# Optimization experiments

Hardware: AMD Instinct MI355X
Metric: run time of the kernel (lower is better)

Reference implementation:

```python
import jax, jax.numpy as jnp
import numpy as np

# SSD300 common_params
MAP_SIZES = np.array([38, 19, 10, 5, 3, 1])
NUM_BOXES = np.array([4, 6, 6, 6, 4, 4])
NUM_OFFSET = 4
LOC_VAR = 0.1
NUM_CLASSES = 21
NEG_POS_RATIO = 3
_counts = MAP_SIZES ** 2 * NUM_BOXES
LAYER_OFFSETS = np.concatenate([[0], np.cumsum(_counts)])[:6]
TOTAL_ANCHORS = int(_counts.sum())  # 8732

B, MAXGT, SEG_HW = 32, 64, 300


def setup_inputs() -> dict:
    key = jax.random.key(0)
    ks = jax.random.split(key, 6)
    rng = np.random.default_rng(0)
    layer = rng.integers(0, 6, (B, MAXGT))
    pos = rng.integers(0, MAP_SIZES[layer] ** 2)
    dbox = rng.integers(0, NUM_BOXES[layer])
    nvalid = rng.integers(8, MAXGT + 1, (B,))
    live = np.arange(MAXGT)[None, :] < nvalid[:, None]
    layer = np.where(live, layer, -100)  # -100 sentinel terminates per-image list
    idx_batch = jnp.asarray(np.stack([np.zeros_like(layer), layer, pos, dbox], -1), dtype=jnp.int64)
    cls_batch = jnp.asarray(rng.integers(1, NUM_CLASSES, (B, MAXGT)), dtype=jnp.int64)
    return {
        "Loc": jax.random.normal(ks[0], (B, TOTAL_ANCHORS, NUM_OFFSET), jnp.float32),
        "Cls": jax.random.normal(ks[1], (B, TOTAL_ANCHORS, NUM_CLASSES), jnp.float32),
        "Seg": jax.random.normal(ks[2], (B, NUM_CLASSES, SEG_HW, SEG_HW), jnp.float32),
        "gt_box_batch": jax.random.uniform(ks[3], (B, MAXGT, NUM_OFFSET), jnp.float32),
        "df_box_batch": jax.random.uniform(ks[4], (B, MAXGT, NUM_OFFSET), jnp.float32),
        "idx_batch": idx_batch,
        "cls_batch": cls_batch,
        "bat_s": B,
        "mining": 1,
        "seg_label": jax.random.randint(ks[5], (B, SEG_HW, SEG_HW), 0, NUM_CLASSES, jnp.int64),
    }


def _build_targets(idx_batch, cls_batch, gt_box_batch, df_box_batch, mining):
    # Vectorized replacement of the nested scalar-scatter loop.
    layer = idx_batch[..., 1]
    fpos = idx_batch[..., 2]
    dbox = idx_batch[..., 3]
    # original loop breaks at first -100: mask everything after it
    valid = jnp.cumprod((layer != -100).astype(jnp.int32), axis=1).astype(bool)
    lc = jnp.clip(layer, 0, 5)
    offs = jnp.asarray(LAYER_OFFSETS)[lc]
    nb = jnp.asarray(NUM_BOXES)[lc]
    # [B, num_boxes, H, W] permuted to [B, H, W, num_boxes] -> flat = pos*nb + dbox
    flat = offs + fpos * nb + dbox
    flat = jnp.where(valid, flat, TOTAL_ANCHORS)  # dump slot
    bsz = idx_batch.shape[0]
    b_idx = jnp.arange(bsz)[:, None]
    init = -1 if mining else 0
    cls_t = jnp.full((bsz, TOTAL_ANCHORS + 1), init, dtype=jnp.int32)
    cls_t = cls_t.at[b_idx, flat].set(jnp.where(valid, cls_batch.astype(jnp.int32), init))
    delta = (gt_box_batch - df_box_batch) / LOC_VAR
    loc_t = jnp.zeros((bsz, TOTAL_ANCHORS + 1, NUM_OFFSET), jnp.float32)
    loc_t = loc_t.at[b_idx, flat].set(jnp.where(valid[..., None], delta, 0.0))
    return cls_t[:, :TOTAL_ANCHORS], loc_t[:, :TOTAL_ANCHORS]


def _mt_loss(Loc, Cls, Seg, gt_box_batch, df_box_batch, idx_batch, cls_batch, mining, seg_label):
    cls_t, loc_t = _build_targets(idx_batch, cls_batch, gt_box_batch, df_box_batch, mining)
    pos = cls_t > 0
    num_pos = jnp.maximum(pos.sum(), 1).astype(jnp.float32)
    logp = jax.nn.log_softmax(Cls, axis=-1)  # [B,N,C]
    ce = -jnp.take_along_axis(logp, jnp.clip(cls_t, 0, NUM_CLASSES - 1)[..., None].astype(jnp.int32), axis=-1)[..., 0]
    loss_cls_pos = jnp.where(pos, ce, 0.0).sum()
    if mining:
        # hard negative mining: top (3*num_pos_i) background losses per image
        ce_bg = -logp[..., 0]
        neg_cand = cls_t == -1
        scores = jnp.where(neg_cand, ce_bg, -jnp.inf)
        order = jnp.argsort(-scores, axis=1)
        rank = jnp.argsort(order, axis=1)
        num_pos_i = pos.sum(axis=1, keepdims=True)
        num_neg_i = jnp.minimum(NEG_POS_RATIO * num_pos_i, neg_cand.sum(axis=1, keepdims=True))
        sel = neg_cand & (rank < num_neg_i)
        loss_cls_neg = jnp.where(sel, ce_bg, 0.0).sum()
    else:
        # all non-positive anchors are explicit background targets (cls_t == 0)
        loss_cls_neg = jnp.where(~pos, ce, 0.0).sum()
    loss_cls = (loss_cls_pos + loss_cls_neg) / num_pos
    d = Loc - loc_t
    ad = jnp.abs(d)
    sl1 = jnp.where(ad < 1.0, 0.5 * d * d, ad - 0.5)
    loss_loc = jnp.where(pos[..., None], sl1, 0.0).sum() / num_pos
    seg_logp = jax.nn.log_softmax(Seg, axis=1)  # [B,C,H,W]
    seg_ce = -jnp.take_along_axis(seg_logp, seg_label[:, None].astype(jnp.int32), axis=1)[:, 0]
    loss_seg = seg_ce.mean()
    return loss_cls + loss_loc + loss_seg


def reference(Loc, Cls, Seg, gt_box_batch, df_box_batch, idx_batch, cls_batch, bat_s, mining, seg_label):
    return _mt_loss(Loc, Cls, Seg, gt_box_batch, df_box_batch, idx_batch, cls_batch, mining, seg_label)
```

## Files before the change

kernel.cpp:

```cpp
#include <hip/hip_runtime.h>
#include <stdint.h>

#define BATCH 32
#define NA 8732
#define NC 21
#define SHW 90000
#define MAXGT 64
#define NQ (SHW / 4)

#define SPI 8
#define SQUADS 2816
#define QPT 11
#define WQ 704
#define CHBF (SQUADS * 4)
#define CSTEP ((size_t)NQ * 16)

__constant__ int c_loff[6] = {0, 5776, 7942, 8542, 8692, 8728};
__constant__ int c_lnb[6]  = {4, 6, 6, 6, 4, 4};

__device__ __forceinline__ unsigned f2key(float f) {
    unsigned u = __float_as_uint(f);
    return (u & 0x80000000u) ? ~u : (u | 0x80000000u);
}
__device__ __forceinline__ float key2f(unsigned k) {
    return __uint_as_float((k & 0x80000000u) ? (k ^ 0x80000000u) : ~k);
}

__global__ __launch_bounds__(64) void k_init(float* __restrict__ acc, int* __restrict__ npt,
                                             unsigned* __restrict__ done) {
    int t = threadIdx.x;
    if (t < 8) acc[t] = 0.0f;
    if (t == 8) *npt = 0;
    if (t == 9) *done = 0u;
}

__global__ __launch_bounds__(1024) void k_build(
    const int* __restrict__ idxb, const int* __restrict__ clsb,
    const float* __restrict__ gt, const float* __restrict__ df,
    const float* __restrict__ Loc, const int* __restrict__ mining_p,
    signed char* __restrict__ cls_t, float* __restrict__ acc,
    int* __restrict__ num_pos_i, int* __restrict__ neg_cnt_i,
    int* __restrict__ npt)
{
    const int b = blockIdx.x;
    const int tid = threadIdx.x;
    __shared__ int s_flat[MAXGT];
    __shared__ int s_cls[MAXGT];
    __shared__ float s_delta[MAXGT][4];
    __shared__ int s_nv;
    __shared__ float s_wf[16];
    __shared__ int s_wp[16];
    __shared__ int s_wn[16];

    if (tid < MAXGT) {
        int layer = idxb[(b * MAXGT + tid) * 4 + 1];
        int fpos  = idxb[(b * MAXGT + tid) * 4 + 2];
        int dbox  = idxb[(b * MAXGT + tid) * 4 + 3];
        int fl;
        if (layer == -100) fl = -2;
        else {
            int lc = min(max(layer, 0), 5);
            fl = c_loff[lc] + fpos * c_lnb[lc] + dbox;
        }
        s_flat[tid] = fl;
        s_cls[tid] = clsb[b * MAXGT + tid];
        #pragma unroll
        for (int o = 0; o < 4; o++)
            s_delta[tid][o] = (gt[(b * MAXGT + tid) * 4 + o] - df[(b * MAXGT + tid) * 4 + o]) / 0.1f;
    }
    __syncthreads();
    if (tid == 0) {
        int nv = MAXGT;
        for (int j = 0; j < MAXGT; j++) if (s_flat[j] == -2) { nv = j; break; }
        s_nv = nv;
    }
    __syncthreads();
    const int nv = s_nv;

    int rflat[MAXGT];
    #pragma unroll
    for (int j = 0; j < MAXGT; j++)
        rflat[j] = (j < nv) ? s_flat[j] : -3;

    const int mining = *mining_p;
    const signed char cinit = mining ? (signed char)(-1) : (signed char)0;
    int pos_cnt = 0, neg_cnt = 0;
    float loc_sum = 0.0f;

    for (int a = tid; a < NA; a += 1024) {
        int best = -1;
        #pragma unroll
        for (int j = 0; j < MAXGT; j++)
            best = (rflat[j] == a) ? j : best;
        signed char cv = cinit;
        if (best >= 0) cv = (signed char)s_cls[best];
        cls_t[b * NA + a] = cv;
        if (cv > 0) {
            pos_cnt++;
            const float4 l4 = *reinterpret_cast<const float4*>(Loc + ((size_t)b * NA + a) * 4);
            float lv[4] = {l4.x, l4.y, l4.z, l4.w};
            #pragma unroll
            for (int o = 0; o < 4; o++) {
                float d = lv[o] - s_delta[best][o];
                float ad = fabsf(d);
                loc_sum += (ad < 1.0f) ? (0.5f * d * d) : (ad - 0.5f);
            }
        } else if (cv == -1) {
            neg_cnt++;
        }
    }

    #pragma unroll
    for (int d = 32; d > 0; d >>= 1) {
        loc_sum += __shfl_down(loc_sum, d);
        pos_cnt += __shfl_down(pos_cnt, d);
        neg_cnt += __shfl_down(neg_cnt, d);
    }
    const int lane = tid & 63, wv = tid >> 6;
    if (lane == 0) { s_wf[wv] = loc_sum; s_wp[wv] = pos_cnt; s_wn[wv] = neg_cnt; }
    __syncthreads();
    if (tid == 0) {
        float lf = 0.0f; int pp = 0, nn = 0;
        #pragma unroll
        for (int w = 0; w < 16; w++) { lf += s_wf[w]; pp += s_wp[w]; nn += s_wn[w]; }
        atomicAdd(acc + 2, lf);
        num_pos_i[b] = pp;
        atomicAdd(npt, pp);
        neg_cnt_i[b] = nn;
    }
}

__global__ __launch_bounds__(256) void k_cls(
    const float* __restrict__ Cls, const signed char* __restrict__ cls_t,
    const int* __restrict__ mining_p, float* __restrict__ scores,
    float* __restrict__ acc)
{
    __shared__ __align__(16) float s_c[256 * NC];
    __shared__ float s_wp[4];
    __shared__ float s_wn[4];
    const int t = threadIdx.x;
    const size_t base = (size_t)blockIdx.x * (256 * NC);
    const size_t total = (size_t)BATCH * NA * NC;
    const int nchunks = (int)((total - base) >> 2) < (256 * NC / 4)
                        ? (int)((total - base) >> 2) : (256 * NC / 4);
    #pragma unroll
    for (int k = 0; k < 6; k++) {
        int j4 = t + k * 256;
        if (j4 < nchunks) {
            *reinterpret_cast<float4*>(&s_c[j4 * 4]) =
                *reinterpret_cast<const float4*>(Cls + base + (size_t)j4 * 4);
        }
    }
    __syncthreads();

    const int r = blockIdx.x * 256 + t;
    const int mining = *mining_p;
    float pos_ce = 0.0f, neg_ce = 0.0f;
    if (r < BATCH * NA) {
        float f[NC];
        #pragma unroll
        for (int c = 0; c < NC; c++) f[c] = s_c[t * NC + c];
        float m = f[0];
        #pragma unroll
        for (int c = 1; c < NC; c++) m = fmaxf(m, f[c]);
        float s = 0.0f;
        #pragma unroll
        for (int c = 0; c < NC; c++) s += __expf(f[c] - m);
        float lse = m + __logf(s);
        int ct = (int)cls_t[r];
        int lab = ct > 0 ? ct : 0;
        float xt = f[0];
        #pragma unroll
        for (int c = 1; c < NC; c++) xt = (c == lab) ? f[c] : xt;
        float ce_bg = lse - f[0];
        if (ct > 0) pos_ce = lse - xt;
        if (mining) {
            scores[r] = (ct == -1) ? ce_bg : -__builtin_inff();
        } else if (ct <= 0) {
            neg_ce = ce_bg;
        }
    }
    #pragma unroll
    for (int d = 32; d > 0; d >>= 1) {
        pos_ce += __shfl_down(pos_ce, d);
        neg_ce += __shfl_down(neg_ce, d);
    }
    const int lane = t & 63, wv = t >> 6;
    if (lane == 0) { s_wp[wv] = pos_ce; s_wn[wv] = neg_ce; }
    __syncthreads();
    if (t == 0) {
        float p = s_wp[0] + s_wp[1] + s_wp[2] + s_wp[3];
        float n = s_wn[0] + s_wn[1] + s_wn[2] + s_wn[3];
        if (p != 0.0f) atomicAdd(acc + 0, p);
        if (n != 0.0f) atomicAdd(acc + 1, n);
    }
}

__global__ __launch_bounds__(256) void k_topk(
    const float* __restrict__ scores, const int* __restrict__ num_pos_i,
    const int* __restrict__ neg_cnt_i, const int* __restrict__ mining_p,
    float* __restrict__ acc)
{
    if (*mining_p == 0) return;
    const int b = blockIdx.x;
    const int tid = threadIdx.x;
    const int k = min(3 * num_pos_i[b], neg_cnt_i[b]);
    if (k <= 0) return;

    __shared__ unsigned s_keys[NA];
    __shared__ int s_hist[256];
    __shared__ int s_wsum[4];
    __shared__ int s_selb;
    __shared__ int s_sele;
    __shared__ float s_wf[4];
    __shared__ int s_wc[4];

    const float* sc = scores + (size_t)b * NA;
    for (int a = tid; a < NA; a += 256)
        s_keys[a] = f2key(sc[a]);

    const int lane = tid & 63, wv = tid >> 6;
    unsigned pref = 0u;
    int k_rem = k;

    #pragma unroll
    for (int lvl = 0; lvl < 4; lvl++) {
        const int sh = 24 - lvl * 8;
        s_hist[tid] = 0;
        __syncthreads();
        for (int a = tid; a < NA; a += 256) {
            unsigned key = s_keys[a];
            bool in = (lvl == 0) || ((key >> (sh + 8)) == pref);
            if (in) atomicAdd(&s_hist[(key >> sh) & 0xFF], 1);
        }
        __syncthreads();
        const int b_rev = 255 - tid;
        const int v = s_hist[b_rev];
        int x = v;
        #pragma unroll
        for (int d = 1; d < 64; d <<= 1) {
            int o = __shfl_up(x, d);
            if (lane >= d) x += o;
        }
        if (lane == 63) s_wsum[wv] = x;
        __syncthreads();
        for (int w = 0; w < wv; w++) x += s_wsum[w];
        if (x >= k_rem && (x - v) < k_rem) { s_selb = b_rev; s_sele = x - v; }
        __syncthreads();
        pref = (pref << 8) | (unsigned)s_selb;
        k_rem -= s_sele;
        __syncthreads();
    }

    float sum_g = 0.0f; int cnt_g = 0;
    for (int a = tid; a < NA; a += 256) {
        unsigned key = s_keys[a];
        if (key > pref) { sum_g += key2f(key); cnt_g++; }
    }
    #pragma unroll
    for (int d = 32; d > 0; d >>= 1) {
        sum_g += __shfl_down(sum_g, d);
        cnt_g += __shfl_down(cnt_g, d);
    }
    if (lane == 0) { s_wf[wv] = sum_g; s_wc[wv] = cnt_g; }
    __syncthreads();
    if (tid == 0) {
        float sg = s_wf[0] + s_wf[1] + s_wf[2] + s_wf[3];
        int cg = s_wc[0] + s_wc[1] + s_wc[2] + s_wc[3];
        atomicAdd(acc + 1, sg + (float)(k - cg) * key2f(pref));
    }
}


__device__ __forceinline__ void upd1(float& m, float& s, float& tg,
                                     int lab, float x, int c) {
    tg = (lab == c) ? x : tg;
    const float d = x - m;
    const float e = __expf(-fabsf(d));
    s = (d > 0.0f) ? fmaf(s, e, 1.0f) : (s + e);
    m = fmaxf(m, x);
}
__device__ __forceinline__ void upd4p(float4& m, float4& s, float4& tg,
                                      unsigned lp, const float4& x, int c) {
    upd1(m.x, s.x, tg.x, (int)(lp & 0xFFu),         x.x, c);
    upd1(m.y, s.y, tg.y, (int)((lp >> 8) & 0xFFu),  x.y, c);
    upd1(m.z, s.z, tg.z, (int)((lp >> 16) & 0xFFu), x.z, c);
    upd1(m.w, s.w, tg.w, (int)((lp >> 24) & 0xFFu), x.w, c);
}

#define GLOAD_I4(dst, addr) \
    asm volatile("global_load_dwordx4 %0, %1, off" : "=v"(dst) : "v"(addr))
#define SWAIT(lit) do { \
    asm volatile("s_waitcnt vmcnt(" #lit ")" ::: "memory"); \
    __builtin_amdgcn_sched_barrier(0); } while (0)

__device__ __forceinline__ void stage_chan(const char* segbase, int c,
                                           float* ldswave, const uint32_t* boff) {
    const char* cb = segbase + (size_t)c * CSTEP;
    #pragma unroll
    for (int i = 0; i < QPT; i++) {
        __builtin_amdgcn_global_load_lds(
            (__attribute__((address_space(1))) void*)(cb + boff[i]),
            (__attribute__((address_space(3))) void*)(ldswave + i * 256),
            16, 0, 0);
    }
}

#define RBAR() do { \
    __builtin_amdgcn_sched_barrier(0); \
    __builtin_amdgcn_s_barrier(); \
    __builtin_amdgcn_sched_barrier(0); } while (0)

__global__ __launch_bounds__(256, 1) void k_seg(
    const float* __restrict__ Seg, const int* __restrict__ slab_lab,
    float* __restrict__ acc, const int* __restrict__ npt,
    unsigned* __restrict__ done, float* __restrict__ out)
{
    __shared__ __align__(16) float s_buf[3 * CHBF];
    __shared__ float s_w[4];
    const int t = threadIdx.x;
    const int lane = t & 63, w = t >> 6;
    const int img = blockIdx.x >> 3;
    const int sl  = blockIdx.x & 7;
    const int qbase = sl * SQUADS;

    const char* segbase = (const char*)(Seg + (size_t)img * NC * SHW);
    const char* labbase = (const char*)(slab_lab + (size_t)img * SHW);

    int4 la[QPT];
    #pragma unroll
    for (int k = 0; k < QPT; k++) {
        int q = qbase + t + k * 256;
        int qc = (q < NQ) ? q : (NQ - 1);
        GLOAD_I4(la[k], (uint64_t)labbase + (uint64_t)qc * 16u);
    }
    SWAIT(0);
    unsigned lp[QPT];
    #pragma unroll
    for (int k = 0; k < QPT; k++)
        lp[k] = ((unsigned)la[k].x & 0xFFu) | (((unsigned)la[k].y & 0xFFu) << 8)
              | (((unsigned)la[k].z & 0xFFu) << 16) | (((unsigned)la[k].w & 0xFFu) << 24);

    uint32_t boff[QPT];
    #pragma unroll
    for (int i = 0; i < QPT; i++) {
        int qg = qbase + w * WQ + i * 64 + lane;
        int qc = (qg < NQ) ? qg : (NQ - 1);
        boff[i] = (uint32_t)qc * 16u;
    }
    float* ldsw0 = s_buf + (size_t)w * (WQ * 4);

    float4 m4[QPT], s4[QPT], t4[QPT];

    stage_chan(segbase, 0, ldsw0, boff);
    stage_chan(segbase, 1, ldsw0 + CHBF, boff);
    SWAIT(11);
    RBAR();
    stage_chan(segbase, 2, ldsw0 + 2 * CHBF, boff);
    #pragma unroll
    for (int k = 0; k < QPT; k++) {
        float4 x = *reinterpret_cast<const float4*>(s_buf + (size_t)(t + k * 256) * 4);
        m4[k] = x; t4[k] = x;
        s4[k] = make_float4(1.f, 1.f, 1.f, 1.f);
    }

    #pragma unroll 1
    for (int c = 1; c < NC; ++c) {
        if (c == NC - 1) SWAIT(0); else SWAIT(11);
        RBAR();
        if (c + 2 < NC) stage_chan(segbase, c + 2, ldsw0 + ((c + 2) % 3) * CHBF, boff);
        const float* bp = s_buf + (size_t)(c % 3) * CHBF;
        #pragma unroll
        for (int k = 0; k < QPT; k++) {
            float4 x = *reinterpret_cast<const float4*>(bp + (size_t)(t + k * 256) * 4);
            upd4p(m4[k], s4[k], t4[k], lp[k], x, c);
        }
    }

    float lsum = 0.0f;
    #pragma unroll
    for (int k = 0; k < QPT; k++) {
        int q = qbase + t + k * 256;
        if (q < NQ) {
            lsum += (m4[k].x + __logf(s4[k].x) - t4[k].x)
                  + (m4[k].y + __logf(s4[k].y) - t4[k].y)
                  + (m4[k].z + __logf(s4[k].z) - t4[k].z)
                  + (m4[k].w + __logf(s4[k].w) - t4[k].w);
        }
    }

    #pragma unroll
    for (int d = 32; d > 0; d >>= 1) lsum += __shfl_down(lsum, d);
    if (lane == 0) s_w[w] = lsum;
    __syncthreads();
    if (t == 0) {
        atomicAdd(acc + 3, s_w[0] + s_w[1] + s_w[2] + s_w[3]);
        __threadfence();
        unsigned old = atomicAdd(done, 1u);
        if (old == gridDim.x - 1) {
            __threadfence();
            int np_i = *npt;
            float np = (float)(np_i > 1 ? np_i : 1);
            out[0] = (acc[0] + acc[1] + acc[2]) / np
                   + acc[3] / (float)(BATCH * SHW);
        }
    }
}

extern "C" void kernel_launch(void* const* d_in, const int* in_sizes, int n_in,
                              void* d_out, int out_size, void* d_ws, size_t ws_size,
                              hipStream_t stream)
{
    const float* Loc = (const float*)d_in[0];
    const float* Cls = (const float*)d_in[1];
    const float* Seg = (const float*)d_in[2];
    const float* gt  = (const float*)d_in[3];
    const float* df  = (const float*)d_in[4];
    const int* idxb  = (const int*)d_in[5];
    const int* clsb  = (const int*)d_in[6];
    const int* mining_p = (const int*)d_in[8];
    const int* slab  = (const int*)d_in[9];
    float* out = (float*)d_out;

    char* ws = (char*)d_ws;
    float* acc        = (float*)ws;
    int*   npt        = (int*)(ws + 32);
    unsigned* done    = (unsigned*)(ws + 36);
    int*   num_pos_i  = (int*)(ws + 64);
    int*   neg_cnt_i  = (int*)(ws + 192);
    signed char* cls_t = (signed char*)(ws + 512);
    float* scores      = (float*)(ws + 512 + 279424);

    hipLaunchKernelGGL(k_init, dim3(1), dim3(64), 0, stream, acc, npt, done);
    hipLaunchKernelGGL(k_build, dim3(BATCH), dim3(1024), 0, stream,
                       idxb, clsb, gt, df, Loc, mining_p, cls_t, acc, num_pos_i, neg_cnt_i, npt);
    hipLaunchKernelGGL(k_cls, dim3((BATCH * NA + 255) / 256), dim3(256), 0, stream,
                       Cls, cls_t, mining_p, scores, acc);
    hipLaunchKernelGGL(k_topk, dim3(BATCH), dim3(256), 0, stream,
                       scores, num_pos_i, neg_cnt_i, mining_p, acc);
    hipLaunchKernelGGL(k_seg, dim3(BATCH * SPI), dim3(256), 0, stream,
                       Seg, slab, acc, npt, done, out);
}
```

Before: 124.5 us.

## Restructure seg kernel into small slabs looping over image groups with 4-deep LDS pipeline

Each of the 256 seg blocks now handles a 768-quad slab for 4 images in sequence instead of one large 2816-quad slab of a single image. Per-thread register state shrinks from 11 to 3 quads, and channel staging uses a 4-slot LDS ring with three channels in flight instead of a 3-slot ring. The aim is lower register pressure and deeper memory prefetch. The cost is a pipeline restart and refill for every image, plus an extra barrier per image.

```diff
diff --git a/kernel.cpp b/kernel.cpp
--- a/kernel.cpp
+++ b/kernel.cpp
@@ -8,11 +8,12 @@
 #define MAXGT 64
 #define NQ (SHW / 4)
 
-#define SPI 8
-#define SQUADS 2816
-#define QPT 11
-#define WQ 704
-#define CHBF (SQUADS * 4)
+#define GRP 4
+#define IPG 8
+#define NSL 32
+#define SQ2 768
+#define KQ 3
+#define CHB (SQ2 * 4)
 #define CSTEP ((size_t)NQ * 16)
 
 __constant__ int c_loff[6] = {0, 5776, 7942, 8542, 8692, 8728};
@@ -294,99 +295,109 @@
     asm volatile("s_waitcnt vmcnt(" #lit ")" ::: "memory"); \
     __builtin_amdgcn_sched_barrier(0); } while (0)
 
-__device__ __forceinline__ void stage_chan(const char* segbase, int c,
-                                           float* ldswave, const uint32_t* boff) {
-    const char* cb = segbase + (size_t)c * CSTEP;
-    #pragma unroll
-    for (int i = 0; i < QPT; i++) {
-        __builtin_amdgcn_global_load_lds(
-            (__attribute__((address_space(1))) void*)(cb + boff[i]),
-            (__attribute__((address_space(3))) void*)(ldswave + i * 256),
-            16, 0, 0);
-    }
-}
-
 #define RBAR() do { \
     __builtin_amdgcn_sched_barrier(0); \
     __builtin_amdgcn_s_barrier(); \
     __builtin_amdgcn_sched_barrier(0); } while (0)
+
+__device__ __forceinline__ void stage_chan(const char* segbase, int c,
+                                           float* ldsslot, int w,
+                                           const uint32_t* boff) {
+    const char* cb = segbase + (size_t)c * CSTEP;
+    #pragma unroll
+    for (int i = 0; i < 3; i++) {
+        __builtin_amdgcn_global_load_lds(
+            (__attribute__((address_space(1))) void*)(cb + boff[i]),
+            (__attribute__((address_space(3))) void*)(ldsslot + (w * 3 + i) * 256),
+            16, 0, 0);
+    }
+}
 
 __global__ __launch_bounds__(256, 1) void k_seg(
     const float* __restrict__ Seg, const int* __restrict__ slab_lab,
     float* __restrict__ acc, const int* __restrict__ npt,
     unsigned* __restrict__ done, float* __restrict__ out)
 {
-    __shared__ __align__(16) float s_buf[3 * CHBF];
+    __shared__ __align__(16) float s_buf[4 * CHB];
     __shared__ float s_w[4];
     const int t = threadIdx.x;
     const int lane = t & 63, w = t >> 6;
-    const int img = blockIdx.x >> 3;
-    const int sl  = blockIdx.x & 7;
-    const int qbase = sl * SQUADS;
-
-    const char* segbase = (const char*)(Seg + (size_t)img * NC * SHW);
-    const char* labbase = (const char*)(slab_lab + (size_t)img * SHW);
-
-    int4 la[QPT];
-    #pragma unroll
-    for (int k = 0; k < QPT; k++) {
-        int q = qbase + t + k * 256;
-        int qc = (q < NQ) ? q : (NQ - 1);
-        GLOAD_I4(la[k], (uint64_t)labbase + (uint64_t)qc * 16u);
-    }
-    SWAIT(0);
-    unsigned lp[QPT];
-    #pragma unroll
-    for (int k = 0; k < QPT; k++)
-        lp[k] = ((unsigned)la[k].x & 0xFFu) | (((unsigned)la[k].y & 0xFFu) << 8)
-              | (((unsigned)la[k].z & 0xFFu) << 16) | (((unsigned)la[k].w & 0xFFu) << 24);
-
-    uint32_t boff[QPT];
-    #pragma unroll
-    for (int i = 0; i < QPT; i++) {
-        int qg = qbase + w * WQ + i * 64 + lane;
+    const int slab = blockIdx.x & 31;
+    const int i8   = blockIdx.x >> 5;
+    const int qbase = slab * SQ2;
+
+    uint32_t boff[3];
+    #pragma unroll
+    for (int i = 0; i < 3; i++) {
+        int qg = qbase + (w * 3 + i) * 64 + lane;
         int qc = (qg < NQ) ? qg : (NQ - 1);
         boff[i] = (uint32_t)qc * 16u;
     }
-    float* ldsw0 = s_buf + (size_t)w * (WQ * 4);
-
-    float4 m4[QPT], s4[QPT], t4[QPT];
-
-    stage_chan(segbase, 0, ldsw0, boff);
-    stage_chan(segbase, 1, ldsw0 + CHBF, boff);
-    SWAIT(11);
-    RBAR();
-    stage_chan(segbase, 2, ldsw0 + 2 * CHBF, boff);
-    #pragma unroll
-    for (int k = 0; k < QPT; k++) {
-        float4 x = *reinterpret_cast<const float4*>(s_buf + (size_t)(t + k * 256) * 4);
-        m4[k] = x; t4[k] = x;
-        s4[k] = make_float4(1.f, 1.f, 1.f, 1.f);
-    }
+
+    float lsum = 0.0f;
 
     #pragma unroll 1
-    for (int c = 1; c < NC; ++c) {
-        if (c == NC - 1) SWAIT(0); else SWAIT(11);
+    for (int g = 0; g < GRP; ++g) {
+        const int img = i8 + g * IPG;
+        const char* segbase = (const char*)Seg + (size_t)img * NC * SHW * 4;
+        const char* labbase = (const char*)slab_lab + (size_t)img * SHW * 4;
+
+        int4 la[KQ];
+        #pragma unroll
+        for (int k = 0; k < KQ; k++) {
+            int q = qbase + t + k * 256;
+            int qc = (q < NQ) ? q : (NQ - 1);
+            GLOAD_I4(la[k], (uint64_t)labbase + (uint64_t)qc * 16u);
+        }
+        SWAIT(0);
+        unsigned lp[KQ];
+        #pragma unroll
+        for (int k = 0; k < KQ; k++)
+            lp[k] = ((unsigned)la[k].x & 0xFFu) | (((unsigned)la[k].y & 0xFFu) << 8)
+                  | (((unsigned)la[k].z & 0xFFu) << 16) | (((unsigned)la[k].w & 0xFFu) << 24);
+
+        stage_chan(segbase, 0, s_buf + 0 * CHB, w, boff);
+        stage_chan(segbase, 1, s_buf + 1 * CHB, w, boff);
+        stage_chan(segbase, 2, s_buf + 2 * CHB, w, boff);
+        stage_chan(segbase, 3, s_buf + 3 * CHB, w, boff);
+        SWAIT(9);
         RBAR();
-        if (c + 2 < NC) stage_chan(segbase, c + 2, ldsw0 + ((c + 2) % 3) * CHBF, boff);
-        const float* bp = s_buf + (size_t)(c % 3) * CHBF;
-        #pragma unroll
-        for (int k = 0; k < QPT; k++) {
-            float4 x = *reinterpret_cast<const float4*>(bp + (size_t)(t + k * 256) * 4);
-            upd4p(m4[k], s4[k], t4[k], lp[k], x, c);
-        }
-    }
-
-    float lsum = 0.0f;
-    #pragma unroll
-    for (int k = 0; k < QPT; k++) {
-        int q = qbase + t + k * 256;
-        if (q < NQ) {
-            lsum += (m4[k].x + __logf(s4[k].x) - t4[k].x)
-                  + (m4[k].y + __logf(s4[k].y) - t4[k].y)
-                  + (m4[k].z + __logf(s4[k].z) - t4[k].z)
-                  + (m4[k].w + __logf(s4[k].w) - t4[k].w);
-        }
+
+        float4 m4[KQ], s4[KQ], t4[KQ];
+        #pragma unroll
+        for (int k = 0; k < KQ; k++) {
+            float4 x = *reinterpret_cast<const float4*>(s_buf + (size_t)(t + k * 256) * 4);
+            m4[k] = x; t4[k] = x;
+            s4[k] = make_float4(1.f, 1.f, 1.f, 1.f);
+        }
+
+        #pragma unroll 1
+        for (int c = 1; c < NC; ++c) {
+            if (c <= NC - 3)      SWAIT(6);
+            else if (c == NC - 2) SWAIT(3);
+            else                  SWAIT(0);
+            RBAR();
+            if (c + 3 < NC)
+                stage_chan(segbase, c + 3, s_buf + ((c + 3) & 3) * CHB, w, boff);
+            const float* bp = s_buf + (size_t)(c & 3) * CHB;
+            #pragma unroll
+            for (int k = 0; k < KQ; k++) {
+                float4 x = *reinterpret_cast<const float4*>(bp + (size_t)(t + k * 256) * 4);
+                upd4p(m4[k], s4[k], t4[k], lp[k], x, c);
+            }
+        }
+
+        #pragma unroll
+        for (int k = 0; k < KQ; k++) {
+            int q = qbase + t + k * 256;
+            if (q < NQ) {
+                lsum += (m4[k].x + __logf(s4[k].x) - t4[k].x)
+                      + (m4[k].y + __logf(s4[k].y) - t4[k].y)
+                      + (m4[k].z + __logf(s4[k].z) - t4[k].z)
+                      + (m4[k].w + __logf(s4[k].w) - t4[k].w);
+            }
+        }
+        RBAR();
     }
 
     #pragma unroll
@@ -438,6 +449,6 @@
                        Cls, cls_t, mining_p, scores, acc);
     hipLaunchKernelGGL(k_topk, dim3(BATCH), dim3(256), 0, stream,
                        scores, num_pos_i, neg_cnt_i, mining_p, acc);
-    hipLaunchKernelGGL(k_seg, dim3(BATCH * SPI), dim3(256), 0, stream,
+    hipLaunchKernelGGL(k_seg, dim3(256), dim3(256), 0, stream,
                        Seg, slab, acc, npt, done, out);
 }
```

Result: slower. 151.1 us (+21.3%).
